# Kernel tuning notes

Hardware: AMD Instinct MI355X
Metric: run time of the kernel (lower is better)

Reference implementation:

```python
import jax, jax.numpy as jnp
import numpy as np

BN_EPS = 1e-5


def setup_inputs() -> dict:
    key = jax.random.key(0)
    k1, k2, k3, k4, k5 = jax.random.split(key, 5)
    B, N, K, C_in, C_out = 8, 8192, 16, 64, 64
    x = jax.random.normal(k1, (B, N, C_in), dtype=jnp.float32)
    knn = jax.random.randint(k2, (B, N, K), 0, N, dtype=jnp.int64)
    # learned params: linear weight (out, in), BN affine params.
    # NOTE: module inits bn.weight to `init`=0.0 which would zero the output;
    # we use random gamma so the baseline exercises nontrivial math.
    W = jax.random.normal(k3, (C_out, C_in), dtype=jnp.float32) * (1.0 / np.sqrt(C_in))
    gamma = jax.random.normal(k4, (C_out,), dtype=jnp.float32) * 0.1 + 1.0
    beta = jax.random.normal(k5, (C_out,), dtype=jnp.float32) * 0.1
    return {"x": x, "knn": knn, "W": W, "gamma": gamma, "beta": beta}


def reference(x, knn, W, gamma, beta):
    B, N, C = x.shape
    # linear projection (no bias): [B,N,C_in] x [C_out,C_in] -> [B,N,C_out]
    h = jnp.einsum('bnc,oc->bno', x, W)
    # KNN gather + mean aggregation: agg[b,n] = mean_k h[b, knn[b,n,k]]
    agg = jax.vmap(lambda hb, kb: hb[kb])(h, knn).mean(axis=2)  # [B,N,C_out]
    # BatchNorm1d in training mode over B*N tokens (biased variance)
    flat = agg.reshape(B * N, -1)
    mu = flat.mean(axis=0)
    var = flat.var(axis=0)
    out = (flat - mu) * jax.lax.rsqrt(var + BN_EPS) * gamma + beta
    return out.reshape(B, N, -1)
```

## Files before the change

### kernel.cpp

```cpp
#include <hip/hip_runtime.h>

#define BB 8
#define NN 8192
#define KK 16
#define CC 64
#define TPB 64
#define THREADS 256
#define BPB (NN / TPB)
#define NBLK (BB * BPB)
#define NTOK (BB * NN)
#define BN_EPS 1e-5f

__global__ __launch_bounds__(THREADS) void k_fused_gather(
    const float* __restrict__ x, const int* __restrict__ knn,
    const float* __restrict__ W, float* __restrict__ agg,
    float* __restrict__ partials)
{
    __shared__ float sWt[CC][CC];
    __shared__ float sAgg[TPB][CC + 4];
    __shared__ float sRed[2][16][CC];

    const int tid   = threadIdx.x;
    const int batch = blockIdx.x & 7;
    const int chunk = blockIdx.x >> 3;
    const int n_base = chunk * TPB;

    for (int i = tid; i < CC * CC; i += THREADS) {
        const int o = i >> 6, c = i & 63;
        sWt[c][o] = W[i];
    }

    const int g = tid >> 4;
    const int l = tid & 15;
    const float4* __restrict__ x4 = (const float4*)x;

    for (int it = 0; it < TPB / 16; ++it) {
        const int t = it * 16 + g;
        const int n = n_base + t;
        const int idx_my = knn[(batch * NN + n) * KK + l];
        float sx = 0.f, sy = 0.f, sz = 0.f, sw = 0.f;
        #pragma unroll
        for (int k = 0; k < KK; ++k) {
            const int idx = __shfl(idx_my, k, 16);
            const float4 v = x4[(size_t)(batch * NN + idx) * (CC / 4) + l];
            sx += v.x; sy += v.y; sz += v.z; sw += v.w;
        }
        const float inv = 1.0f / KK;
        *(float4*)&sAgg[t][l * 4] = make_float4(sx * inv, sy * inv, sz * inv, sw * inv);
    }
    __syncthreads();

    const int tq = tid >> 4;
    const int oq = tid & 15;
    float acc[4][4] = {};
    #pragma unroll
    for (int c4 = 0; c4 < CC; c4 += 4) {
        float av[4][4], wv[4][4];
        #pragma unroll
        for (int t = 0; t < 4; ++t) {
            const float4 tmp = *(const float4*)&sAgg[tq * 4 + t][c4];
            av[t][0] = tmp.x; av[t][1] = tmp.y; av[t][2] = tmp.z; av[t][3] = tmp.w;
        }
        #pragma unroll
        for (int cc = 0; cc < 4; ++cc) {
            const float4 tmp = *(const float4*)&sWt[c4 + cc][oq * 4];
            wv[cc][0] = tmp.x; wv[cc][1] = tmp.y; wv[cc][2] = tmp.z; wv[cc][3] = tmp.w;
        }
        #pragma unroll
        for (int t = 0; t < 4; ++t)
            #pragma unroll
            for (int cc = 0; cc < 4; ++cc)
                #pragma unroll
                for (int o = 0; o < 4; ++o)
                    acc[t][o] += av[t][cc] * wv[cc][o];
    }

    float4* __restrict__ agg4 = (float4*)agg;
    float ps[4] = {}, pq[4] = {};
    #pragma unroll
    for (int t = 0; t < 4; ++t) {
        const int n = n_base + tq * 4 + t;
        agg4[(size_t)(batch * NN + n) * (CC / 4) + oq] =
            make_float4(acc[t][0], acc[t][1], acc[t][2], acc[t][3]);
        #pragma unroll
        for (int o = 0; o < 4; ++o) {
            ps[o] += acc[t][o];
            pq[o] += acc[t][o] * acc[t][o];
        }
    }
    #pragma unroll
    for (int o = 0; o < 4; ++o) {
        sRed[0][tq][oq * 4 + o] = ps[o];
        sRed[1][tq][oq * 4 + o] = pq[o];
    }
    __syncthreads();
    if (tid < 128) {
        const int w = tid >> 6, c = tid & 63;
        float s = 0.f;
        #pragma unroll
        for (int i = 0; i < 16; ++i) s += sRed[w][i][c];
        partials[blockIdx.x * 128 + tid] = s;
    }
}

__global__ __launch_bounds__(128) void k_reduce1(
    const float* __restrict__ partials, float* __restrict__ p2)
{
    const int tid = threadIdx.x;
    const int j = blockIdx.x;
    float s = 0.f;
    #pragma unroll
    for (int i = 0; i < NBLK / 64; ++i)
        s += partials[(size_t)(j * (NBLK / 64) + i) * 128 + tid];
    p2[j * 128 + tid] = s;
}

__global__ __launch_bounds__(128) void k_stats(
    const float* __restrict__ p2, const float* __restrict__ gamma,
    const float* __restrict__ beta, float* __restrict__ ss)
{
    __shared__ float tot[128];
    const int tid = threadIdx.x;
    float s = 0.f;
    #pragma unroll
    for (int j = 0; j < 64; ++j) s += p2[j * 128 + tid];
    tot[tid] = s;
    __syncthreads();
    if (tid < CC) {
        const float invn = 1.0f / (float)NTOK;
        const float mu  = tot[tid] * invn;
        const float var = tot[64 + tid] * invn - mu * mu;
        const float sc  = gamma[tid] * rsqrtf(var + BN_EPS);
        ss[tid]      = sc;
        ss[CC + tid] = beta[tid] - mu * sc;
    }
}

__global__ __launch_bounds__(256) void k_norm(
    float* __restrict__ out, const float* __restrict__ ss)
{
    const int idx = blockIdx.x * 256 + threadIdx.x;
    const float4 a  = ((const float4*)out)[idx];
    const int c4 = idx & (CC / 4 - 1);
    const float4 sc = ((const float4*)ss)[c4];
    const float4 sh = ((const float4*)ss)[CC / 4 + c4];
    ((float4*)out)[idx] = make_float4(
        fmaf(a.x, sc.x, sh.x), fmaf(a.y, sc.y, sh.y),
        fmaf(a.z, sc.z, sh.z), fmaf(a.w, sc.w, sh.w));
}

extern "C" void kernel_launch(void* const* d_in, const int* in_sizes, int n_in,
                              void* d_out, int out_size, void* d_ws, size_t ws_size,
                              hipStream_t stream)
{
    const float* x     = (const float*)d_in[0];
    const int*   knn   = (const int*)d_in[1];
    const float* W     = (const float*)d_in[2];
    const float* gamma = (const float*)d_in[3];
    const float* beta  = (const float*)d_in[4];
    float* out = (float*)d_out;

    float* partials = (float*)d_ws;
    float* p2       = partials + NBLK * 128;
    float* ss       = p2 + 64 * 128;

    k_fused_gather<<<NBLK, THREADS, 0, stream>>>(x, knn, W, out, partials);
    k_reduce1<<<64, 128, 0, stream>>>(partials, p2);
    k_stats<<<1, 128, 0, stream>>>(p2, gamma, beta, ss);
    k_norm<<<out_size / 4 / 256, 256, 0, stream>>>(out, ss);
}
```

Before: 39.46 us.

## Fuse gather, BN stats and normalize into one cooperative persistent kernel

Replaces the four-kernel pipeline with a single cooperative grid kernel that computes the gathered projections, writes per-chunk partial sums in a transposed layout, and reduces them after a grid barrier. The last chunk of each block stays in registers and is normalized directly, so its intermediate is never written to and reread from memory. The goal is to remove launch gaps and the separate reduction and normalize passes. In exchange it adds two grid-wide syncs, per-call host queries of device properties and occupancy, and a fallback path for when cooperative launch is unavailable.

```diff
diff --git a/kernel.cpp b/kernel.cpp
--- a/kernel.cpp
+++ b/kernel.cpp
@@ -1,4 +1,9 @@
 #include <hip/hip_runtime.h>
+#include <hip/hip_cooperative_groups.h>
+
+namespace cg = cooperative_groups;
+
+typedef float f4 __attribute__((ext_vector_type(4)));
 
 #define BB 8
 #define NN 8192
@@ -6,64 +11,57 @@
 #define CC 64
 #define TPB 64
 #define THREADS 256
-#define BPB (NN / TPB)
-#define NBLK (BB * BPB)
+#define NCHUNK 1024
 #define NTOK (BB * NN)
 #define BN_EPS 1e-5f
 
-__global__ __launch_bounds__(THREADS) void k_fused_gather(
-    const float* __restrict__ x, const int* __restrict__ knn,
-    const float* __restrict__ W, float* __restrict__ agg,
-    float* __restrict__ partials)
-{
-    __shared__ float sWt[CC][CC];
-    __shared__ float sAgg[TPB][CC + 4];
-    __shared__ float sRed[2][16][CC];
-
-    const int tid   = threadIdx.x;
-    const int batch = blockIdx.x & 7;
-    const int chunk = blockIdx.x >> 3;
-    const int n_base = chunk * TPB;
-
-    for (int i = tid; i < CC * CC; i += THREADS) {
-        const int o = i >> 6, c = i & 63;
-        sWt[c][o] = W[i];
-    }
-
-    const int g = tid >> 4;
-    const int l = tid & 15;
-    const float4* __restrict__ x4 = (const float4*)x;
-
-    for (int it = 0; it < TPB / 16; ++it) {
+__device__ __forceinline__ void process_chunk(
+    int ch, const f4* __restrict__ x4, const int* __restrict__ knn,
+    const float (*sWt)[CC], float (*uagg)[CC + 4], float (*ured)[16][CC],
+    float* __restrict__ partials, float acc[4][4])
+{
+    const int tid = threadIdx.x;
+    const int g = tid >> 4, l = tid & 15;
+    const int batch = ch & 7;
+    const int nb = (ch >> 3) * TPB;
+
+    __syncthreads();
+
+    #pragma unroll
+    for (int it = 0; it < 4; ++it) {
         const int t = it * 16 + g;
-        const int n = n_base + t;
-        const int idx_my = knn[(batch * NN + n) * KK + l];
+        const int idx_my =
+            __builtin_nontemporal_load(&knn[(batch * NN + nb + t) * KK + l]);
         float sx = 0.f, sy = 0.f, sz = 0.f, sw = 0.f;
         #pragma unroll
         for (int k = 0; k < KK; ++k) {
             const int idx = __shfl(idx_my, k, 16);
-            const float4 v = x4[(size_t)(batch * NN + idx) * (CC / 4) + l];
+            const f4 v = x4[(size_t)(batch * NN + idx) * (CC / 4) + l];
             sx += v.x; sy += v.y; sz += v.z; sw += v.w;
         }
         const float inv = 1.0f / KK;
-        *(float4*)&sAgg[t][l * 4] = make_float4(sx * inv, sy * inv, sz * inv, sw * inv);
-    }
-    __syncthreads();
-
-    const int tq = tid >> 4;
-    const int oq = tid & 15;
-    float acc[4][4] = {};
+        f4 r; r.x = sx * inv; r.y = sy * inv; r.z = sz * inv; r.w = sw * inv;
+        *(f4*)&uagg[t][l * 4] = r;
+    }
+    __syncthreads();
+
+    const int tq = tid >> 4, oq = tid & 15;
+    #pragma unroll
+    for (int t = 0; t < 4; ++t)
+        #pragma unroll
+        for (int o = 0; o < 4; ++o) acc[t][o] = 0.f;
+
     #pragma unroll
     for (int c4 = 0; c4 < CC; c4 += 4) {
         float av[4][4], wv[4][4];
         #pragma unroll
         for (int t = 0; t < 4; ++t) {
-            const float4 tmp = *(const float4*)&sAgg[tq * 4 + t][c4];
+            const f4 tmp = *(const f4*)&uagg[tq * 4 + t][c4];
             av[t][0] = tmp.x; av[t][1] = tmp.y; av[t][2] = tmp.z; av[t][3] = tmp.w;
         }
         #pragma unroll
         for (int cc = 0; cc < 4; ++cc) {
-            const float4 tmp = *(const float4*)&sWt[c4 + cc][oq * 4];
+            const f4 tmp = *(const f4*)&sWt[c4 + cc][oq * 4];
             wv[cc][0] = tmp.x; wv[cc][1] = tmp.y; wv[cc][2] = tmp.z; wv[cc][3] = tmp.w;
         }
         #pragma unroll
@@ -74,79 +72,189 @@
                 for (int o = 0; o < 4; ++o)
                     acc[t][o] += av[t][cc] * wv[cc][o];
     }
-
-    float4* __restrict__ agg4 = (float4*)agg;
+    __syncthreads();
+
     float ps[4] = {}, pq[4] = {};
     #pragma unroll
-    for (int t = 0; t < 4; ++t) {
-        const int n = n_base + tq * 4 + t;
-        agg4[(size_t)(batch * NN + n) * (CC / 4) + oq] =
-            make_float4(acc[t][0], acc[t][1], acc[t][2], acc[t][3]);
+    for (int t = 0; t < 4; ++t)
         #pragma unroll
         for (int o = 0; o < 4; ++o) {
             ps[o] += acc[t][o];
             pq[o] += acc[t][o] * acc[t][o];
         }
-    }
     #pragma unroll
     for (int o = 0; o < 4; ++o) {
-        sRed[0][tq][oq * 4 + o] = ps[o];
-        sRed[1][tq][oq * 4 + o] = pq[o];
+        ured[0][tq][oq * 4 + o] = ps[o];
+        ured[1][tq][oq * 4 + o] = pq[o];
     }
     __syncthreads();
     if (tid < 128) {
         const int w = tid >> 6, c = tid & 63;
         float s = 0.f;
         #pragma unroll
-        for (int i = 0; i < 16; ++i) s += sRed[w][i][c];
-        partials[blockIdx.x * 128 + tid] = s;
-    }
-}
-
-__global__ __launch_bounds__(128) void k_reduce1(
-    const float* __restrict__ partials, float* __restrict__ p2)
-{
+        for (int i = 0; i < 16; ++i) s += ured[w][i][c];
+        __builtin_nontemporal_store(s, &partials[(size_t)tid * NCHUNK + ch]);
+    }
+}
+
+__global__ __launch_bounds__(THREADS, 4) void k_coop(
+    const float* __restrict__ x, const int* __restrict__ knn,
+    const float* __restrict__ W, const float* __restrict__ gamma,
+    const float* __restrict__ beta, float* __restrict__ out,
+    float* __restrict__ partials, float* __restrict__ ss)
+{
+    __shared__ float sWt[CC][CC];
+    __shared__ union { float agg[TPB][CC + 4]; float red[2][16][CC]; } u;
+    __shared__ float sFin[8];
+
+    const int tid = threadIdx.x;
+    const int R = gridDim.x;
+    for (int i = tid; i < CC * CC; i += THREADS) sWt[i & 63][i >> 6] = W[i];
+
+    const int tq = tid >> 4, oq = tid & 15;
+    f4* out4 = (f4*)out;
+    float acc[4][4];
+
+    for (int ch = blockIdx.x + R; ch < NCHUNK; ch += R) {
+        process_chunk(ch, (const f4*)x, knn, sWt, u.agg, u.red, partials, acc);
+        const int batch = ch & 7, nb = (ch >> 3) * TPB;
+        #pragma unroll
+        for (int t = 0; t < 4; ++t) {
+            f4 r; r.x = acc[t][0]; r.y = acc[t][1]; r.z = acc[t][2]; r.w = acc[t][3];
+            out4[(size_t)(batch * NN + nb + tq * 4 + t) * (CC / 4) + oq] = r;
+        }
+    }
+    process_chunk(blockIdx.x, (const f4*)x, knn, sWt, u.agg, u.red, partials, acc);
+
+    __threadfence();
+    cg::this_grid().sync();
+
+    if (blockIdx.x < 64) {
+        const int j = blockIdx.x;
+        float s1 = 0.f, s2 = 0.f;
+        for (int i = tid; i < NCHUNK; i += THREADS) {
+            s1 += partials[j * NCHUNK + i];
+            s2 += partials[(64 + j) * NCHUNK + i];
+        }
+        #pragma unroll
+        for (int off = 32; off; off >>= 1) {
+            s1 += __shfl_down(s1, off);
+            s2 += __shfl_down(s2, off);
+        }
+        if ((tid & 63) == 0) { sFin[tid >> 6] = s1; sFin[4 + (tid >> 6)] = s2; }
+        __syncthreads();
+        if (tid == 0) {
+            const float S1 = sFin[0] + sFin[1] + sFin[2] + sFin[3];
+            const float S2 = sFin[4] + sFin[5] + sFin[6] + sFin[7];
+            const float invn = 1.0f / (float)NTOK;
+            const float mu  = S1 * invn;
+            const float var = S2 * invn - mu * mu;
+            const float sc  = gamma[j] * rsqrtf(var + BN_EPS);
+            ss[j]      = sc;
+            ss[CC + j] = beta[j] - mu * sc;
+        }
+    }
+    __threadfence();
+    cg::this_grid().sync();
+
+    const f4 sc4 = ((const f4*)ss)[oq];
+    const f4 sh4 = ((const f4*)ss)[CC / 4 + oq];
+    {
+        const int batch = blockIdx.x & 7, nb = (blockIdx.x >> 3) * TPB;
+        #pragma unroll
+        for (int t = 0; t < 4; ++t) {
+            f4 r;
+            r.x = fmaf(acc[t][0], sc4.x, sh4.x);
+            r.y = fmaf(acc[t][1], sc4.y, sh4.y);
+            r.z = fmaf(acc[t][2], sc4.z, sh4.z);
+            r.w = fmaf(acc[t][3], sc4.w, sh4.w);
+            __builtin_nontemporal_store(
+                r, &out4[(size_t)(batch * NN + nb + tq * 4 + t) * (CC / 4) + oq]);
+        }
+    }
+    for (int ch = blockIdx.x + R; ch < NCHUNK; ch += R) {
+        const int batch = ch & 7, nb = (ch >> 3) * TPB;
+        #pragma unroll
+        for (int t = 0; t < 4; ++t) {
+            const size_t ix = (size_t)(batch * NN + nb + tq * 4 + t) * (CC / 4) + oq;
+            const f4 a = out4[ix];
+            f4 r;
+            r.x = fmaf(a.x, sc4.x, sh4.x);
+            r.y = fmaf(a.y, sc4.y, sh4.y);
+            r.z = fmaf(a.z, sc4.z, sh4.z);
+            r.w = fmaf(a.w, sc4.w, sh4.w);
+            __builtin_nontemporal_store(r, &out4[ix]);
+        }
+    }
+}
+
+__global__ __launch_bounds__(THREADS, 4) void k_fb_main(
+    const float* __restrict__ x, const int* __restrict__ knn,
+    const float* __restrict__ W, float* __restrict__ out,
+    float* __restrict__ partials)
+{
+    __shared__ float sWt[CC][CC];
+    __shared__ union { float agg[TPB][CC + 4]; float red[2][16][CC]; } u;
+    const int tid = threadIdx.x;
+    for (int i = tid; i < CC * CC; i += THREADS) sWt[i & 63][i >> 6] = W[i];
+    float acc[4][4];
+    process_chunk(blockIdx.x, (const f4*)x, knn, sWt, u.agg, u.red, partials, acc);
+    const int tq = tid >> 4, oq = tid & 15;
+    const int batch = blockIdx.x & 7, nb = (blockIdx.x >> 3) * TPB;
+    f4* out4 = (f4*)out;
+    #pragma unroll
+    for (int t = 0; t < 4; ++t) {
+        f4 r; r.x = acc[t][0]; r.y = acc[t][1]; r.z = acc[t][2]; r.w = acc[t][3];
+        out4[(size_t)(batch * NN + nb + tq * 4 + t) * (CC / 4) + oq] = r;
+    }
+}
+
+__global__ __launch_bounds__(THREADS) void k_fb_stats(
+    const float* __restrict__ partials, const float* __restrict__ gamma,
+    const float* __restrict__ beta, float* __restrict__ ss)
+{
+    __shared__ float sFin[8];
     const int tid = threadIdx.x;
     const int j = blockIdx.x;
-    float s = 0.f;
-    #pragma unroll
-    for (int i = 0; i < NBLK / 64; ++i)
-        s += partials[(size_t)(j * (NBLK / 64) + i) * 128 + tid];
-    p2[j * 128 + tid] = s;
-}
-
-__global__ __launch_bounds__(128) void k_stats(
-    const float* __restrict__ p2, const float* __restrict__ gamma,
-    const float* __restrict__ beta, float* __restrict__ ss)
-{
-    __shared__ float tot[128];
-    const int tid = threadIdx.x;
-    float s = 0.f;
-    #pragma unroll
-    for (int j = 0; j < 64; ++j) s += p2[j * 128 + tid];
-    tot[tid] = s;
-    __syncthreads();
-    if (tid < CC) {
+    float s1 = 0.f, s2 = 0.f;
+    for (int i = tid; i < NCHUNK; i += THREADS) {
+        s1 += partials[j * NCHUNK + i];
+        s2 += partials[(64 + j) * NCHUNK + i];
+    }
+    #pragma unroll
+    for (int off = 32; off; off >>= 1) {
+        s1 += __shfl_down(s1, off);
+        s2 += __shfl_down(s2, off);
+    }
+    if ((tid & 63) == 0) { sFin[tid >> 6] = s1; sFin[4 + (tid >> 6)] = s2; }
+    __syncthreads();
+    if (tid == 0) {
+        const float S1 = sFin[0] + sFin[1] + sFin[2] + sFin[3];
+        const float S2 = sFin[4] + sFin[5] + sFin[6] + sFin[7];
         const float invn = 1.0f / (float)NTOK;
-        const float mu  = tot[tid] * invn;
-        const float var = tot[64 + tid] * invn - mu * mu;
-        const float sc  = gamma[tid] * rsqrtf(var + BN_EPS);
-        ss[tid]      = sc;
-        ss[CC + tid] = beta[tid] - mu * sc;
-    }
-}
-
-__global__ __launch_bounds__(256) void k_norm(
+        const float mu  = S1 * invn;
+        const float var = S2 * invn - mu * mu;
+        const float sc  = gamma[j] * rsqrtf(var + BN_EPS);
+        ss[j]      = sc;
+        ss[CC + j] = beta[j] - mu * sc;
+    }
+}
+
+__global__ __launch_bounds__(256) void k_fb_norm(
     float* __restrict__ out, const float* __restrict__ ss)
 {
     const int idx = blockIdx.x * 256 + threadIdx.x;
-    const float4 a  = ((const float4*)out)[idx];
+    f4* out4 = (f4*)out;
+    const f4 a  = out4[idx];
     const int c4 = idx & (CC / 4 - 1);
-    const float4 sc = ((const float4*)ss)[c4];
-    const float4 sh = ((const float4*)ss)[CC / 4 + c4];
-    ((float4*)out)[idx] = make_float4(
-        fmaf(a.x, sc.x, sh.x), fmaf(a.y, sc.y, sh.y),
-        fmaf(a.z, sc.z, sh.z), fmaf(a.w, sc.w, sh.w));
+    const f4 sc = ((const f4*)ss)[c4];
+    const f4 sh = ((const f4*)ss)[CC / 4 + c4];
+    f4 r;
+    r.x = fmaf(a.x, sc.x, sh.x);
+    r.y = fmaf(a.y, sc.y, sh.y);
+    r.z = fmaf(a.z, sc.z, sh.z);
+    r.w = fmaf(a.w, sc.w, sh.w);
+    __builtin_nontemporal_store(r, &out4[idx]);
 }
 
 extern "C" void kernel_launch(void* const* d_in, const int* in_sizes, int n_in,
@@ -161,11 +269,36 @@
     float* out = (float*)d_out;
 
     float* partials = (float*)d_ws;
-    float* p2       = partials + NBLK * 128;
-    float* ss       = p2 + 64 * 128;
-
-    k_fused_gather<<<NBLK, THREADS, 0, stream>>>(x, knn, W, out, partials);
-    k_reduce1<<<64, 128, 0, stream>>>(partials, p2);
-    k_stats<<<1, 128, 0, stream>>>(p2, gamma, beta, ss);
-    k_norm<<<out_size / 4 / 256, 256, 0, stream>>>(out, ss);
-}
+    float* ss       = partials + 128 * NCHUNK;
+
+    int R = 0;
+    {
+        int dev = 0;
+        (void)hipGetDevice(&dev);
+        hipDeviceProp_t prop;
+        if (hipGetDeviceProperties(&prop, dev) == hipSuccess && prop.cooperativeLaunch) {
+            int maxB = 0;
+            if (hipOccupancyMaxActiveBlocksPerMultiprocessor(&maxB, k_coop, THREADS, 0)
+                    == hipSuccess && maxB > 0) {
+                int r = maxB * prop.multiProcessorCount;
+                if (r > NCHUNK) r = NCHUNK;
+                r &= ~7;
+                if (r >= 768) R = r;
+            }
+        }
+    }
+
+    if (R > 0) {
+        void* args[] = {
+            (void*)&x, (void*)&knn, (void*)&W, (void*)&gamma, (void*)&beta,
+            (void*)&out, (void*)&partials, (void*)&ss
+        };
+        if (hipLaunchCooperativeKernel((void*)k_coop, dim3(R), dim3(THREADS),
+                                       args, 0, stream) == hipSuccess)
+            return;
+    }
+
+    k_fb_main<<<NCHUNK, THREADS, 0, stream>>>(x, knn, W, out, partials);
+    k_fb_stats<<<64, THREADS, 0, stream>>>(partials, gamma, beta, ss);
+    k_fb_norm<<<(NTOK * CC) / 4 / 256, 256, 0, stream>>>(out, ss);
+}
```

After: 43.28 us. 1.1x slower.
